# Optimization experiments

Hardware: AMD Instinct MI355X
Metric: run time of the kernel (lower is better)

Reference implementation:

```python
import jax, jax.numpy as jnp
import numpy as np

# Forest-Ruth symplectic coefficients
THETA = 1.0 / (2.0 - 2.0 ** (1.0 / 3.0))
C1 = THETA / 2.0
C2 = (1.0 - THETA) / 2.0
C3 = (1.0 - THETA) / 2.0
C4 = THETA / 2.0
D1 = THETA
D2 = 1.0 - 2.0 * THETA
D3 = THETA
DT = 0.01          # self.dt
DT_SCALE = 1.0
PI = np.float32(np.pi)


def _wrap_torus(x):
    # topology_id == 1: wrap coordinates onto the torus [-pi, pi)
    return (x + PI) % (2.0 * PI) - PI


def setup_inputs() -> dict:
    key = jax.random.key(0)
    k0, k1, k2, k3, k4 = jax.random.split(key, 5)
    B, D, K = 32768, 512, 64
    x = jax.random.normal(k0, (B, D), jnp.float32)
    v = jax.random.normal(k1, (B, D), jnp.float32)
    force = 0.1 * jax.random.normal(k2, (B, D), jnp.float32)
    U = 0.05 * jax.random.normal(k3, (D, K), jnp.float32)  # low-rank Christoffel factor
    W = 0.05 * jax.random.normal(k4, (K, D), jnp.float32)
    return {"x": x, "v": v, "force": force, "U": U, "W": W, "steps": 4}


def reference(x, v, force, U, W, steps):
    dt = DT * DT_SCALE

    def acceleration(tx, tv):
        # Christoffel contraction Gamma^i_{jk} v^j v^k with low-rank Gamma = U (.)^2 W
        h = tv @ U                 # [B, K]
        christ = (h * h) @ W       # [B, D]
        return -christ + force     # a = -Gamma(v,v) + external force

    cx, cv = x, v
    for _ in range(steps):
        x1 = _wrap_torus(cx + C1 * dt * cv)
        v1 = cv + D1 * dt * acceleration(x1, cv)
        x2 = _wrap_torus(x1 + C2 * dt * v1)
        v2 = v1 + D2 * dt * acceleration(x2, v1)
        x3 = _wrap_torus(x2 + C3 * dt * v2)
        v3 = v2 + D3 * dt * acceleration(x3, v2)
        cx, cv = _wrap_torus(x3 + C4 * dt * v3), v3
    return (cx, cv)
```

## Files before the change

### kernel.cpp

```cpp
#include <hip/hip_runtime.h>


#define D_DIM 512
#define ROWS  64
#define VSTR  516
#define HSTR  65
#define NTH   1024
#define LDS_BYTES ((ROWS*VSTR + ROWS*HSTR) * 4)

__device__ __forceinline__ float wrap_torus(float y) {
    const float PI_F  = 3.14159265358979323846f;
    const float TPI_F = 6.28318530717958647692f;
    float t = y + PI_F;
    if (t >= TPI_F) t -= TPI_F;
    else if (t < 0.0f) t += TPI_F;
    return t - PI_F;
}

__global__ __launch_bounds__(NTH) void fr_kernel(
    const float* __restrict__ xin, const float* __restrict__ vin,
    const float* __restrict__ fin, const float* __restrict__ Um,
    const float* __restrict__ Wm, float* __restrict__ xout,
    float* __restrict__ vout)
{
    extern __shared__ float lds[];
    float* vs = lds;
    float* hs = lds + ROWS * VSTR;

    const int t = threadIdx.x;
    const int l = t & 63;
    const int w = __builtin_amdgcn_readfirstlane(t >> 6);

    const double theta = 1.0 / (2.0 - 1.2599210498948732);
    const float c1dt = (float)(theta * 0.5 * 0.01);
    const float c2dt = (float)((1.0 - theta) * 0.5 * 0.01);
    const float d1dt = (float)(theta * 0.01);
    const float d2dt = (float)((1.0 - 2.0 * theta) * 0.01);

    const int rowBase = (int)blockIdx.x * ROWS;
    const int colBase = w << 5;

    float xv[32], fv[32];
    {
        const float* xg = xin + (size_t)(rowBase + l) * D_DIM + colBase;
        const float* fg = fin + (size_t)(rowBase + l) * D_DIM + colBase;
        #pragma unroll
        for (int q = 0; q < 8; ++q) {
            float4 a = *(const float4*)(xg + 4*q);
            float4 b = *(const float4*)(fg + 4*q);
            xv[4*q+0]=a.x; xv[4*q+1]=a.y; xv[4*q+2]=a.z; xv[4*q+3]=a.w;
            fv[4*q+0]=b.x; fv[4*q+1]=b.y; fv[4*q+2]=b.z; fv[4*q+3]=b.w;
        }
    }
    {
        const float* vg = vin + (size_t)rowBase * D_DIM;
        #pragma unroll
        for (int it = 0; it < 8; ++it) {
            int flat = it*4096 + t*4;
            float4 val = *(const float4*)(vg + flat);
            int row = flat >> 9, col = flat & 511;
            *(float4*)(vs + row*VSTR + col) = val;
        }
    }
    __syncthreads();

    {
        const float* vsl = vs + l*VSTR + colBase;
        #pragma unroll
        for (int q = 0; q < 8; ++q) {
            float4 v4 = *(const float4*)(vsl + 4*q);
            xv[4*q+0] = wrap_torus(xv[4*q+0] + c1dt*v4.x);
            xv[4*q+1] = wrap_torus(xv[4*q+1] + c1dt*v4.y);
            xv[4*q+2] = wrap_torus(xv[4*q+2] + c1dt*v4.z);
            xv[4*q+3] = wrap_torus(xv[4*q+3] + c1dt*v4.w);
        }
    }

    const int kg = (w & 3) << 4;
    const int dg = (w >> 2) << 7;

    #pragma unroll 1
    for (int step = 0; step < 4; ++step) {
      for (int sub = 0; sub < 3; ++sub) {
        const float ddt = (sub == 1) ? d2dt : d1dt;
        const float xc  = (sub == 2) ? c1dt : c2dt;
        const bool dbl  = (sub == 2) && (step < 3);

        __syncthreads();
        for (int i = t; i < ROWS*HSTR; i += NTH) hs[i] = 0.0f;
        __syncthreads();

        {
            float hp[16];
            #pragma unroll
            for (int i = 0; i < 16; ++i) hp[i] = 0.0f;
            const float* vrow = vs + l*VSTR + dg;
            for (int dc = 0; dc < 128; dc += 4) {
                float4 vf = *(const float4*)(vrow + dc);
                float vfa[4] = {vf.x, vf.y, vf.z, vf.w};
                const float* ub = Um + (dg + dc)*64 + kg;
                #pragma unroll
                for (int j = 0; j < 4; ++j) {
                    #pragma unroll
                    for (int ki = 0; ki < 16; ++ki)
                        hp[ki] = fmaf(vfa[j], ub[j*64 + ki], hp[ki]);
                }
            }
            #pragma unroll
            for (int i = 0; i < 16; ++i)
                atomicAdd(hs + l*HSTR + kg + i, hp[i]);
        }
        __syncthreads();

        {
            float acc[32];
            #pragma unroll
            for (int i = 0; i < 32; ++i) acc[i] = 0.0f;
            const float* hrow = hs + l*HSTR;
            for (int k = 0; k < 64; ++k) {
                float hvv = hrow[k];
                float gk = hvv * hvv;
                const float* wb = Wm + (k << 9) + colBase;
                #pragma unroll
                for (int j = 0; j < 32; ++j)
                    acc[j] = fmaf(gk, wb[j], acc[j]);
            }
            float* vsl = vs + l*VSTR + colBase;
            #pragma unroll
            for (int q = 0; q < 8; ++q) {
                float4 vo = *(const float4*)(vsl + 4*q);
                float va[4] = {vo.x, vo.y, vo.z, vo.w};
                #pragma unroll
                for (int c = 0; c < 4; ++c) {
                    int j = 4*q + c;
                    float a  = fv[j] - acc[j];
                    float vn = va[c] + ddt * a;
                    va[c] = vn;
                    float xn = wrap_torus(xv[j] + xc * vn);
                    if (dbl) xn = wrap_torus(xn + c1dt * vn);
                    xv[j] = xn;
                }
                float4 vv; vv.x=va[0]; vv.y=va[1]; vv.z=va[2]; vv.w=va[3];
                *(float4*)(vsl + 4*q) = vv;
            }
        }
      }
    }

    __syncthreads();
    {
        float* xo = xout + (size_t)(rowBase + l) * D_DIM + colBase;
        #pragma unroll
        for (int q = 0; q < 8; ++q) {
            float4 s;
            s.x=xv[4*q+0]; s.y=xv[4*q+1]; s.z=xv[4*q+2]; s.w=xv[4*q+3];
            *(float4*)(xo + 4*q) = s;
        }
    }
    {
        float* vo = vout + (size_t)rowBase * D_DIM;
        #pragma unroll
        for (int it = 0; it < 8; ++it) {
            int flat = it*4096 + t*4;
            int row = flat >> 9, col = flat & 511;
            *(float4*)(vo + flat) = *(const float4*)(vs + row*VSTR + col);
        }
    }
}

extern "C" void kernel_launch(void* const* d_in, const int* in_sizes, int n_in,
                              void* d_out, int out_size, void* d_ws, size_t ws_size,
                              hipStream_t stream) {
    const float* x = (const float*)d_in[0];
    const float* v = (const float*)d_in[1];
    const float* f = (const float*)d_in[2];
    const float* U = (const float*)d_in[3];
    const float* W = (const float*)d_in[4];

    float* xout = (float*)d_out;
    float* vout = xout + (size_t)32768 * 512;

    hipFuncSetAttribute(reinterpret_cast<const void*>(fr_kernel),
                        hipFuncAttributeMaxDynamicSharedMemorySize, LDS_BYTES);
    fr_kernel<<<512, NTH, LDS_BYTES, stream>>>(x, v, f, U, W, xout, vout);
}
```

Baseline: 1.494 ms.

## Replace FP32 FMA matmuls with split-bf16 MFMA and register-resident weights

Rewrites the integrator kernel so both low-rank contractions (v@U and h^2@W) run on bf16 MFMA 32x32x16 instructions. Precision is recovered with a hi/lo bf16 split (three products per tile). A small prep kernel pre-swizzles U and W into MFMA fragment layout in workspace, and each wave keeps its U and W fragments in registers. The state stays in registers in MFMA accumulator layout, with 32 rows per 512-thread block and two blocks per CU. The aim is to remove the scalar FMA bottleneck and the repeated global reads of U and W, at the cost of extra split/pack work, an extra launch, and small accuracy loss from dropping the lo*lo term.

```diff
diff --git a/kernel.cpp b/kernel.cpp
--- a/kernel.cpp
+++ b/kernel.cpp
@@ -1,12 +1,19 @@
 #include <hip/hip_runtime.h>
 
 
-#define D_DIM 512
-#define ROWS  64
-#define VSTR  516
-#define HSTR  65
-#define NTH   1024
-#define LDS_BYTES ((ROWS*VSTR + ROWS*HSTR) * 4)
+#define NTH 512
+
+#define VF0 0
+#define VF1 8192
+#define GF0 16384
+#define GF1 17408
+#define HB  18432
+#define FB  20608
+#define LDS_WORDS 37120
+#define LDS_BYTES (LDS_WORDS*4)
+
+typedef __attribute__((ext_vector_type(8))) short short8;
+typedef __attribute__((ext_vector_type(16))) float float16;
 
 __device__ __forceinline__ float wrap_torus(float y) {
     const float PI_F  = 3.14159265358979323846f;
@@ -17,19 +24,86 @@
     return t - PI_F;
 }
 
-__global__ __launch_bounds__(NTH) void fr_kernel(
+__device__ __forceinline__ void split2(float v, unsigned short& hi, unsigned short& lo) {
+    unsigned u = __float_as_uint(v);
+    unsigned h = (u + 0x7fffu + ((u >> 16) & 1u)) >> 16;
+    hi = (unsigned short)h;
+    float hf = __uint_as_float(h << 16);
+    float r = v - hf;
+    unsigned u2 = __float_as_uint(r);
+    unsigned l = (u2 + 0x7fffu + ((u2 >> 16) & 1u)) >> 16;
+    lo = (unsigned short)l;
+}
+
+__device__ __forceinline__ unsigned pack_split(float v) {
+    unsigned short hi, lo;
+    split2(v, hi, lo);
+    return (((unsigned)hi) << 16) | (unsigned)lo;
+}
+
+__device__ __forceinline__ void unpack_frag(uint4 l4, uint4 h4, short8& fhi, short8& flo) {
+    fhi[0]=(short)(l4.x>>16); flo[0]=(short)(l4.x&0xffffu);
+    fhi[1]=(short)(l4.y>>16); flo[1]=(short)(l4.y&0xffffu);
+    fhi[2]=(short)(l4.z>>16); flo[2]=(short)(l4.z&0xffffu);
+    fhi[3]=(short)(l4.w>>16); flo[3]=(short)(l4.w&0xffffu);
+    fhi[4]=(short)(h4.x>>16); flo[4]=(short)(h4.x&0xffffu);
+    fhi[5]=(short)(h4.y>>16); flo[5]=(short)(h4.y&0xffffu);
+    fhi[6]=(short)(h4.z>>16); flo[6]=(short)(h4.z&0xffffu);
+    fhi[7]=(short)(h4.w>>16); flo[7]=(short)(h4.w&0xffffu);
+}
+
+__global__ void fr_prep(const float* __restrict__ Um, const float* __restrict__ Wm,
+                        unsigned short* __restrict__ usw, unsigned short* __restrict__ wsw) {
+    int tid = blockIdx.x * 256 + threadIdx.x;
+    int lane = tid & 63;
+    if (tid < 4096) {
+        int c   = (tid >> 6) & 7;
+        int ks4 = (tid >> 9) & 3;
+        int nt1 = (tid >> 11) & 1;
+        int fbase = (((nt1 * 4 + ks4) * 8 + c) * 2) * 512;
+        #pragma unroll
+        for (int j = 0; j < 8; ++j) {
+            int d = 128 * ks4 + 16 * c + 8 * (lane >> 5) + j;
+            int n = 32 * nt1 + (lane & 31);
+            unsigned short hi, lo;
+            split2(Um[d * 64 + n], hi, lo);
+            usw[fbase + lane * 8 + j] = hi;
+            usw[fbase + 512 + lane * 8 + j] = lo;
+        }
+    } else {
+        int id = tid - 4096;
+        lane = id & 63;
+        int kk = (id >> 6) & 3;
+        int nt = (id >> 8) & 15;
+        int fbase = ((nt * 4 + kk) * 2) * 512;
+        #pragma unroll
+        for (int j = 0; j < 8; ++j) {
+            int k = 16 * kk + 8 * (lane >> 5) + j;
+            int n = 32 * nt + (lane & 31);
+            unsigned short hi, lo;
+            split2(Wm[k * 512 + n], hi, lo);
+            wsw[fbase + lane * 8 + j] = hi;
+            wsw[fbase + 512 + lane * 8 + j] = lo;
+        }
+    }
+}
+
+__global__ __launch_bounds__(NTH, 2) void fr_mfma(
     const float* __restrict__ xin, const float* __restrict__ vin,
-    const float* __restrict__ fin, const float* __restrict__ Um,
-    const float* __restrict__ Wm, float* __restrict__ xout,
-    float* __restrict__ vout)
+    const float* __restrict__ fin,
+    const short8* __restrict__ usw, const short8* __restrict__ wsw,
+    float* __restrict__ xout, float* __restrict__ vout)
 {
     extern __shared__ float lds[];
-    float* vs = lds;
-    float* hs = lds + ROWS * VSTR;
+    unsigned int* ldsu = (unsigned int*)lds;
 
     const int t = threadIdx.x;
-    const int l = t & 63;
+    const int lane = t & 63;
     const int w = __builtin_amdgcn_readfirstlane(t >> 6);
+    const int nt1 = w & 1;
+    const int ks4 = w >> 1;
+    const int rhalf = lane >> 5;
+    const int R0 = (int)blockIdx.x * 32;
 
     const double theta = 1.0 / (2.0 - 1.2599210498948732);
     const float c1dt = (float)(theta * 0.5 * 0.01);
@@ -37,133 +111,172 @@
     const float d1dt = (float)(theta * 0.01);
     const float d2dt = (float)((1.0 - 2.0 * theta) * 0.01);
 
-    const int rowBase = (int)blockIdx.x * ROWS;
-    const int colBase = w << 5;
-
-    float xv[32], fv[32];
+    short8 Uhi[8], Ulo[8], Whi[2][4], Wlo[2][4];
     {
-        const float* xg = xin + (size_t)(rowBase + l) * D_DIM + colBase;
-        const float* fg = fin + (size_t)(rowBase + l) * D_DIM + colBase;
-        #pragma unroll
-        for (int q = 0; q < 8; ++q) {
-            float4 a = *(const float4*)(xg + 4*q);
-            float4 b = *(const float4*)(fg + 4*q);
-            xv[4*q+0]=a.x; xv[4*q+1]=a.y; xv[4*q+2]=a.z; xv[4*q+3]=a.w;
-            fv[4*q+0]=b.x; fv[4*q+1]=b.y; fv[4*q+2]=b.z; fv[4*q+3]=b.w;
-        }
-    }
+        int ub = ((nt1 * 4 + ks4) * 8) * 2;
+        #pragma unroll
+        for (int c = 0; c < 8; ++c) {
+            Uhi[c] = usw[(ub + 2 * c + 0) * 64 + lane];
+            Ulo[c] = usw[(ub + 2 * c + 1) * 64 + lane];
+        }
+        #pragma unroll
+        for (int nt = 0; nt < 2; ++nt) {
+            int wb = ((w * 2 + nt) * 4) * 2;
+            #pragma unroll
+            for (int kk = 0; kk < 4; ++kk) {
+                Whi[nt][kk] = wsw[(wb + 2 * kk + 0) * 64 + lane];
+                Wlo[nt][kk] = wsw[(wb + 2 * kk + 1) * 64 + lane];
+            }
+        }
+    }
+
+    float vst[2][16], xst[2][16];
+    int cg[2];
+    cg[0] = (w * 2 + 0) * 32 + (lane & 31);
+    cg[1] = (w * 2 + 1) * 32 + (lane & 31);
+    #pragma unroll
+    for (int nt = 0; nt < 2; ++nt) {
+        #pragma unroll
+        for (int r = 0; r < 16; ++r) {
+            int rrow = (r & 3) + 8 * (r >> 2) + 4 * rhalf;
+            size_t idx = (size_t)(R0 + rrow) * 512 + cg[nt];
+            vst[nt][r] = vin[idx];
+            xst[nt][r] = xin[idx];
+        }
+    }
+
     {
-        const float* vg = vin + (size_t)rowBase * D_DIM;
         #pragma unroll
         for (int it = 0; it < 8; ++it) {
-            int flat = it*4096 + t*4;
-            float4 val = *(const float4*)(vg + flat);
+            int flat = it * 2048 + t * 4;
+            float4 val = *(const float4*)(fin + (size_t)R0 * 512 + flat);
             int row = flat >> 9, col = flat & 511;
-            *(float4*)(vs + row*VSTR + col) = val;
-        }
-    }
-    __syncthreads();
-
-    {
-        const float* vsl = vs + l*VSTR + colBase;
-        #pragma unroll
-        for (int q = 0; q < 8; ++q) {
-            float4 v4 = *(const float4*)(vsl + 4*q);
-            xv[4*q+0] = wrap_torus(xv[4*q+0] + c1dt*v4.x);
-            xv[4*q+1] = wrap_torus(xv[4*q+1] + c1dt*v4.y);
-            xv[4*q+2] = wrap_torus(xv[4*q+2] + c1dt*v4.z);
-            xv[4*q+3] = wrap_torus(xv[4*q+3] + c1dt*v4.w);
-        }
-    }
-
-    const int kg = (w & 3) << 4;
-    const int dg = (w >> 2) << 7;
+            *(float4*)(lds + FB + row * 516 + col) = val;
+        }
+    }
+
+    #pragma unroll
+    for (int nt = 0; nt < 2; ++nt)
+        #pragma unroll
+        for (int r = 0; r < 16; ++r)
+            xst[nt][r] = wrap_torus(xst[nt][r] + c1dt * vst[nt][r]);
+
+    #pragma unroll
+    for (int nt = 0; nt < 2; ++nt) {
+        #pragma unroll
+        for (int r = 0; r < 16; ++r) {
+            int m = (r & 3) + 8 * (r >> 2) + 4 * rhalf;
+            int d = cg[nt];
+            unsigned p = pack_split(vst[nt][r]);
+            int kst = d >> 4, lb = (d >> 3) & 1, j = d & 7;
+            ldsu[((j >> 2) ? VF1 : VF0) + (kst * 64 + m + 32 * lb) * 4 + (j & 3)] = p;
+        }
+    }
+    for (int i = t; i < 32 * 68; i += NTH) lds[HB + i] = 0.0f;
 
     #pragma unroll 1
-    for (int step = 0; step < 4; ++step) {
-      for (int sub = 0; sub < 3; ++sub) {
-        const float ddt = (sub == 1) ? d2dt : d1dt;
-        const float xc  = (sub == 2) ? c1dt : c2dt;
-        const bool dbl  = (sub == 2) && (step < 3);
+    for (int sub = 0; sub < 12; ++sub) {
+        const int idx3 = sub - (sub / 3) * 3;
+        const float ddt = (idx3 == 1) ? d2dt : d1dt;
+        const float xc  = (idx3 == 2) ? c1dt : c2dt;
+        const bool dbl  = (idx3 == 2) && (sub != 11);
 
         __syncthreads();
-        for (int i = t; i < ROWS*HSTR; i += NTH) hs[i] = 0.0f;
+
+        float16 acc0, acc1;
+        #pragma unroll
+        for (int i = 0; i < 16; ++i) { acc0[i] = 0.0f; acc1[i] = 0.0f; }
+        #pragma unroll
+        for (int c = 0; c < 8; ++c) {
+            int kst = ks4 * 8 + c;
+            uint4 pl = *(const uint4*)&ldsu[VF0 + (kst * 64 + lane) * 4];
+            uint4 ph = *(const uint4*)&ldsu[VF1 + (kst * 64 + lane) * 4];
+            short8 Ahi, Alo;
+            unpack_frag(pl, ph, Ahi, Alo);
+            acc0 = __builtin_amdgcn_mfma_f32_32x32x16_bf16(Ahi, Uhi[c], acc0, 0, 0, 0);
+            acc1 = __builtin_amdgcn_mfma_f32_32x32x16_bf16(Alo, Uhi[c], acc1, 0, 0, 0);
+            acc1 = __builtin_amdgcn_mfma_f32_32x32x16_bf16(Ahi, Ulo[c], acc1, 0, 0, 0);
+        }
+        {
+            int kcol = nt1 * 32 + (lane & 31);
+            #pragma unroll
+            for (int r = 0; r < 16; ++r) {
+                int m = (r & 3) + 8 * (r >> 2) + 4 * rhalf;
+                atomicAdd(&lds[HB + m * 68 + kcol], acc0[r] + acc1[r]);
+            }
+        }
         __syncthreads();
 
         {
-            float hp[16];
+            int grow = t >> 4;
+            int k4 = (t & 15) * 4;
+            float4 h4 = *(const float4*)&lds[HB + grow * 68 + k4];
+            uint4 gp;
+            gp.x = pack_split(h4.x * h4.x);
+            gp.y = pack_split(h4.y * h4.y);
+            gp.z = pack_split(h4.z * h4.z);
+            gp.w = pack_split(h4.w * h4.w);
+            int kst2 = k4 >> 4, lb2 = (k4 >> 3) & 1, jb = k4 & 7;
+            *(uint4*)&ldsu[((jb >> 2) ? GF1 : GF0) + (kst2 * 64 + grow + 32 * lb2) * 4] = gp;
+        }
+        __syncthreads();
+
+        float16 cA, cB;
+        #pragma unroll
+        for (int i = 0; i < 16; ++i) { cA[i] = 0.0f; cB[i] = 0.0f; }
+        #pragma unroll
+        for (int kk = 0; kk < 4; ++kk) {
+            uint4 pl = *(const uint4*)&ldsu[GF0 + (kk * 64 + lane) * 4];
+            uint4 ph = *(const uint4*)&ldsu[GF1 + (kk * 64 + lane) * 4];
+            short8 Ahi, Alo;
+            unpack_frag(pl, ph, Ahi, Alo);
+            cA = __builtin_amdgcn_mfma_f32_32x32x16_bf16(Ahi, Whi[0][kk], cA, 0, 0, 0);
+            cB = __builtin_amdgcn_mfma_f32_32x32x16_bf16(Ahi, Whi[1][kk], cB, 0, 0, 0);
+            cA = __builtin_amdgcn_mfma_f32_32x32x16_bf16(Alo, Whi[0][kk], cA, 0, 0, 0);
+            cB = __builtin_amdgcn_mfma_f32_32x32x16_bf16(Alo, Whi[1][kk], cB, 0, 0, 0);
+            cA = __builtin_amdgcn_mfma_f32_32x32x16_bf16(Ahi, Wlo[0][kk], cA, 0, 0, 0);
+            cB = __builtin_amdgcn_mfma_f32_32x32x16_bf16(Ahi, Wlo[1][kk], cB, 0, 0, 0);
+        }
+
+        #pragma unroll
+        for (int nt = 0; nt < 2; ++nt) {
             #pragma unroll
-            for (int i = 0; i < 16; ++i) hp[i] = 0.0f;
-            const float* vrow = vs + l*VSTR + dg;
-            for (int dc = 0; dc < 128; dc += 4) {
-                float4 vf = *(const float4*)(vrow + dc);
-                float vfa[4] = {vf.x, vf.y, vf.z, vf.w};
-                const float* ub = Um + (dg + dc)*64 + kg;
+            for (int r = 0; r < 16; ++r) {
+                int m = (r & 3) + 8 * (r >> 2) + 4 * rhalf;
+                float fv = lds[FB + m * 516 + cg[nt]];
+                float christ = (nt == 0) ? cA[r] : cB[r];
+                float vn = vst[nt][r] + ddt * (fv - christ);
+                vst[nt][r] = vn;
+                float xn = wrap_torus(xst[nt][r] + xc * vn);
+                if (dbl) xn = wrap_torus(xn + c1dt * vn);
+                xst[nt][r] = xn;
+            }
+        }
+
+        if (sub != 11) {
+            #pragma unroll
+            for (int nt = 0; nt < 2; ++nt) {
                 #pragma unroll
-                for (int j = 0; j < 4; ++j) {
-                    #pragma unroll
-                    for (int ki = 0; ki < 16; ++ki)
-                        hp[ki] = fmaf(vfa[j], ub[j*64 + ki], hp[ki]);
+                for (int r = 0; r < 16; ++r) {
+                    int m = (r & 3) + 8 * (r >> 2) + 4 * rhalf;
+                    int d = cg[nt];
+                    unsigned p = pack_split(vst[nt][r]);
+                    int kst = d >> 4, lb = (d >> 3) & 1, j = d & 7;
+                    ldsu[((j >> 2) ? VF1 : VF0) + (kst * 64 + m + 32 * lb) * 4 + (j & 3)] = p;
                 }
             }
-            #pragma unroll
-            for (int i = 0; i < 16; ++i)
-                atomicAdd(hs + l*HSTR + kg + i, hp[i]);
-        }
-        __syncthreads();
-
-        {
-            float acc[32];
-            #pragma unroll
-            for (int i = 0; i < 32; ++i) acc[i] = 0.0f;
-            const float* hrow = hs + l*HSTR;
-            for (int k = 0; k < 64; ++k) {
-                float hvv = hrow[k];
-                float gk = hvv * hvv;
-                const float* wb = Wm + (k << 9) + colBase;
-                #pragma unroll
-                for (int j = 0; j < 32; ++j)
-                    acc[j] = fmaf(gk, wb[j], acc[j]);
-            }
-            float* vsl = vs + l*VSTR + colBase;
-            #pragma unroll
-            for (int q = 0; q < 8; ++q) {
-                float4 vo = *(const float4*)(vsl + 4*q);
-                float va[4] = {vo.x, vo.y, vo.z, vo.w};
-                #pragma unroll
-                for (int c = 0; c < 4; ++c) {
-                    int j = 4*q + c;
-                    float a  = fv[j] - acc[j];
-                    float vn = va[c] + ddt * a;
-                    va[c] = vn;
-                    float xn = wrap_torus(xv[j] + xc * vn);
-                    if (dbl) xn = wrap_torus(xn + c1dt * vn);
-                    xv[j] = xn;
-                }
-                float4 vv; vv.x=va[0]; vv.y=va[1]; vv.z=va[2]; vv.w=va[3];
-                *(float4*)(vsl + 4*q) = vv;
-            }
-        }
-      }
-    }
-
-    __syncthreads();
-    {
-        float* xo = xout + (size_t)(rowBase + l) * D_DIM + colBase;
-        #pragma unroll
-        for (int q = 0; q < 8; ++q) {
-            float4 s;
-            s.x=xv[4*q+0]; s.y=xv[4*q+1]; s.z=xv[4*q+2]; s.w=xv[4*q+3];
-            *(float4*)(xo + 4*q) = s;
-        }
-    }
-    {
-        float* vo = vout + (size_t)rowBase * D_DIM;
-        #pragma unroll
-        for (int it = 0; it < 8; ++it) {
-            int flat = it*4096 + t*4;
-            int row = flat >> 9, col = flat & 511;
-            *(float4*)(vo + flat) = *(const float4*)(vs + row*VSTR + col);
+            for (int i = t; i < 32 * 68; i += NTH) lds[HB + i] = 0.0f;
+        }
+    }
+
+    #pragma unroll
+    for (int nt = 0; nt < 2; ++nt) {
+        #pragma unroll
+        for (int r = 0; r < 16; ++r) {
+            int rrow = (r & 3) + 8 * (r >> 2) + 4 * rhalf;
+            size_t idx = (size_t)(R0 + rrow) * 512 + cg[nt];
+            xout[idx] = xst[nt][r];
+            vout[idx] = vst[nt][r];
         }
     }
 }
@@ -180,7 +293,13 @@
     float* xout = (float*)d_out;
     float* vout = xout + (size_t)32768 * 512;
 
-    hipFuncSetAttribute(reinterpret_cast<const void*>(fr_kernel),
+    unsigned short* usw = (unsigned short*)d_ws;
+    unsigned short* wsw = usw + 65536;
+
+    fr_prep<<<32, 256, 0, stream>>>(U, W, usw, wsw);
+
+    hipFuncSetAttribute(reinterpret_cast<const void*>(fr_mfma),
                         hipFuncAttributeMaxDynamicSharedMemorySize, LDS_BYTES);
-    fr_kernel<<<512, NTH, LDS_BYTES, stream>>>(x, v, f, U, W, xout, vout);
-}
+    fr_mfma<<<1024, NTH, LDS_BYTES, stream>>>(
+        x, v, f, (const short8*)usw, (const short8*)wsw, xout, vout);
+}
```

New measurement: 1.225 ms. 1.22x faster.
